# Optimization experiments

Hardware: AMD Instinct MI355X
Metric: run time of the kernel (lower is better)

Reference implementation:

```python
import jax, jax.numpy as jnp
import numpy as np

TWO_PI = 2.0 * np.pi
B, S_IN, S_OUT, K, HID = 1024, 4096, 4096, 8, 512
EPS = 1e-6


def setup_inputs() -> dict:
    key = jax.random.key(0)
    k1, k2, k3, k4, k5, k6, k7, k8 = jax.random.split(key, 8)
    x_in = jax.random.uniform(k1, (B, S_OUT), dtype=jnp.float32) * TWO_PI
    x_passive = jax.random.normal(k2, (B, S_IN), dtype=jnp.float32)
    log_density = jax.random.normal(k3, (B, 1), dtype=jnp.float32)
    # MLP params (nn.Linear default-ish init scale)
    lim1 = 1.0 / np.sqrt(S_IN)
    lim2 = 1.0 / np.sqrt(HID)
    w1 = jax.random.uniform(k4, (S_IN, HID), jnp.float32, -lim1, lim1)
    b1 = jax.random.uniform(k5, (HID,), jnp.float32, -lim1, lim1)
    w2 = jax.random.uniform(k6, (HID, S_OUT * 3 * K), jnp.float32, -lim2, lim2)
    b2 = jax.random.uniform(k7, (S_OUT * 3 * K,), jnp.float32, -lim2, lim2)
    phase_shift = jax.random.uniform(k8, (1,), jnp.float32)
    return {"x_in": x_in, "x_passive": x_passive, "log_density": log_density,
            "w1": w1, "b1": b1, "w2": w2, "b2": b2, "phase_shift": phase_shift}


def reference(x_in, x_passive, log_density, w1, b1, w2, b2, phase_shift):
    # normalise network input with global mean / (unbiased) std, as torch does
    xn = (x_passive - x_passive.mean()) / x_passive.std(ddof=1)
    # dense network: Linear -> tanh -> Linear -> tanh (final_activation=activation)
    net = jnp.tanh(jnp.tanh(xn @ w1 + b1) @ w2 + b2)            # (B, S*3K)
    net = net.reshape(-1, S_OUT, 3 * K)
    h_raw, w_raw, d_raw = net[..., :K], net[..., K:2 * K], net[..., 2 * K:]
    h_norm = jax.nn.softmax(h_raw, axis=2) * TWO_PI              # (B,S,K)
    w_norm = jax.nn.softmax(w_raw, axis=2) * TWO_PI
    d_norm = jax.nn.softplus(d_raw)
    bshape = (h_norm.shape[0], S_OUT, 1)
    x_kp = jnp.concatenate([jnp.full(bshape, -EPS, h_norm.dtype),
                            jnp.cumsum(w_norm, axis=2)], axis=2)  # (B,S,K+1)
    phi_kp = jnp.concatenate([jnp.zeros(bshape, h_norm.dtype),
                              jnp.cumsum(h_norm, axis=2)], axis=2)
    x = x_in[..., None]                                          # (B,S,1)
    # searchsorted (left) per element: count of knots strictly less than x, minus 1
    k_ind = jnp.sum(x_kp < x, axis=2, keepdims=True) - 1         # (B,S,1) int
    k_ind = jnp.clip(k_ind, 0, K - 1)
    g = lambda a, i: jnp.take_along_axis(a, i, axis=2)
    w_k = g(w_norm, k_ind)
    h_k = g(h_norm, k_ind)
    s_k = h_k / w_k
    d_k = g(d_norm, k_ind)
    d_kp1 = g(d_norm, (k_ind + 1) % K)
    x_km1 = g(x_kp, k_ind)
    phi_km1 = g(phi_kp, k_ind)
    alpha = (x - x_km1) / w_k
    a1m = alpha * (1.0 - alpha)
    denom = s_k + (d_kp1 + d_k - 2.0 * s_k) * a1m
    phi_out = (phi_km1 + h_k * (s_k * alpha ** 2 + d_k * a1m) / denom)[..., 0]
    phi_out = (phi_out + phase_shift) % TWO_PI                   # (B,S)
    grad = s_k ** 2 * (d_kp1 * alpha ** 2 + 2.0 * s_k * a1m
                       + d_k * (1.0 - alpha) ** 2) / denom ** 2  # (B,S,1)
    log_density = log_density - jnp.log(grad).sum(axis=1)        # (B,1)
    return phi_out, log_density
```

## Files before the change

### kernel.cpp

```cpp
#include <hip/hip_runtime.h>
#include <cstdint>
#include <cstddef>


typedef unsigned short u16;
typedef __bf16 bf16x8 __attribute__((ext_vector_type(8)));
typedef float f32x4 __attribute__((ext_vector_type(4)));
typedef unsigned short u16x8 __attribute__((ext_vector_type(8)));
typedef unsigned short u16x4 __attribute__((ext_vector_type(4)));
typedef unsigned short u16x2 __attribute__((ext_vector_type(2)));

#define TWOPI_F 6.28318530717958647692f

static __device__ __forceinline__ u16 f32_to_bf16(float f){
  unsigned u = __builtin_bit_cast(unsigned, f);
  return (u16)((u + 0x7fffu + ((u >> 16) & 1u)) >> 16);
}
static __device__ __forceinline__ void async16(void* lds, const void* g){
  __builtin_amdgcn_global_load_lds((const __attribute__((address_space(1))) void*)g,
                                   (__attribute__((address_space(3))) void*)lds,
                                   16, 0, 0);
}
static __device__ __forceinline__ float rcpf(float x){ return __builtin_amdgcn_rcpf(x); }
static __device__ __forceinline__ float fast_tanh(float x){
  x = fminf(fmaxf(x, -15.f), 15.f);
  float e = __expf(2.f * x);
  return (e - 1.f) / (e + 1.f);
}
static __device__ __forceinline__ float tanh_nc(float x){
  const float e2 = __expf(2.f * x);
  return 1.f - 2.f * rcpf(e2 + 1.f);
}
static __device__ __forceinline__ float exp_tanh(float x){
  const float e2 = __expf(2.f * x);
  const float u  = rcpf(e2 + 1.f);
  return __expf(1.f - 2.f * u);
}

__global__ void k_stats(const float* __restrict__ xp, float* __restrict__ stats){
  __shared__ float ss[4], sq[4];
  const int tid = threadIdx.x;
  const long gt = (long)blockIdx.x * 256 + tid;
  const float4* x4 = (const float4*)xp;
  float s = 0.f, q = 0.f;
  #pragma unroll
  for (int p = 0; p < 4; ++p){
    float4 v = x4[gt + (long)p * 262144];
    s += v.x + v.y + v.z + v.w;
    q += v.x*v.x + v.y*v.y + v.z*v.z + v.w*v.w;
  }
  #pragma unroll
  for (int off = 32; off; off >>= 1){
    s += __shfl_down(s, off);
    q += __shfl_down(q, off);
  }
  if ((tid & 63) == 0){ ss[tid>>6] = s; sq[tid>>6] = q; }
  __syncthreads();
  if (tid == 0){
    atomicAdd(stats,     ss[0]+ss[1]+ss[2]+ss[3]);
    atomicAdd(stats + 1, sq[0]+sq[1]+sq[2]+sq[3]);
  }
}

__global__ void k_prep(const float* __restrict__ xp, const float* __restrict__ stats,
                       u16* __restrict__ xn){
  const long t = (long)blockIdx.x * 256 + threadIdx.x;
  const float sum = stats[0], sq = stats[1];
  const float N = 4194304.f;
  const float mean = sum / N;
  const float istd = rsqrtf((sq - sum*sum/N) / (N - 1.f));
  const float4* x4 = (const float4*)xp;
  const float4 a = x4[2*t], b = x4[2*t+1];
  u16x8 o;
  o[0]=f32_to_bf16((a.x-mean)*istd); o[1]=f32_to_bf16((a.y-mean)*istd);
  o[2]=f32_to_bf16((a.z-mean)*istd); o[3]=f32_to_bf16((a.w-mean)*istd);
  o[4]=f32_to_bf16((b.x-mean)*istd); o[5]=f32_to_bf16((b.y-mean)*istd);
  o[6]=f32_to_bf16((b.z-mean)*istd); o[7]=f32_to_bf16((b.w-mean)*istd);
  ((u16x8*)xn)[t] = o;
}

__global__ __launch_bounds__(256) void k_transpose_cvt(const float* __restrict__ in,
                                                       u16* __restrict__ out,
                                                       int Kd, int Nd){
  __shared__ __align__(16) u16 tT[128*256];
  const int tid = threadIdx.x;
  const long k0 = (long)blockIdx.x * 256, n0 = (long)blockIdx.y * 128;
  const int lam = tid & 31, g = tid >> 5;
  const int c = lam * 4;
  const int sig = (lam & 7) << 2;
  #pragma unroll
  for (int pass = 0; pass < 16; ++pass){
    const int P = pass*8 + g;
    const float4 f0 = *(const float4*)&in[(k0 + 2*P    )*Nd + n0 + c];
    const float4 f1 = *(const float4*)&in[(k0 + 2*P + 1)*Nd + n0 + c];
    const int pp = 2*(P ^ sig);
    *(u16x2*)&tT[(c    )*256 + pp] = u16x2{f32_to_bf16(f0.x), f32_to_bf16(f1.x)};
    *(u16x2*)&tT[(c + 1)*256 + pp] = u16x2{f32_to_bf16(f0.y), f32_to_bf16(f1.y)};
    *(u16x2*)&tT[(c + 2)*256 + pp] = u16x2{f32_to_bf16(f0.z), f32_to_bf16(f1.z)};
    *(u16x2*)&tT[(c + 3)*256 + pp] = u16x2{f32_to_bf16(f0.w), f32_to_bf16(f1.w)};
  }
  __syncthreads();
  const int w = tid >> 6, l = tid & 63;
  const int lh = l >> 5, lk = l & 31;
  #pragma unroll
  for (int it = 0; it < 16; ++it){
    const int n = (w << 5) + (it << 1) + lh;
    const int s2 = (n >> 2) & 7;
    const u16x8 v = *(const u16x8*)&tT[n*256 + 8*(lk ^ s2)];
    *(u16x8*)&out[(n0 + n)*Kd + k0 + 8*lk] = v;
  }
}

__global__ __launch_bounds__(256, 2) void k_gemm1(
    const u16* __restrict__ xn,
    const u16* __restrict__ w1t,
    float* __restrict__ pp)
{
  __shared__ __align__(16) u16 sA[4][64*32];
  __shared__ __align__(16) u16 sB[4][64*32];
  const int tid = threadIdx.x, lane = tid & 63, w = tid >> 6;
  const int n0 = blockIdx.x << 6, m0 = blockIdx.y << 6;
  const int ks = blockIdx.z;
  const int wm = w >> 1, wn = w & 1;
  const int rA = lane >> 2, cA = (lane & 3) << 3;
  const int fr = lane & 15, fq = lane >> 4;
  const f32x4 z4 = {0.f, 0.f, 0.f, 0.f};
  f32x4 acc[2][2];
  #pragma unroll
  for (int i=0;i<2;i++){ acc[i][0] = z4; acc[i][1] = z4; }

  auto stage = [&](int kt){
    const int b = kt & 3;
    const int kofs = (ks << 11) + (kt << 5) + cA;
    async16(sA[b] + w*512, xn  + (long)(m0 + w*16 + rA)*4096 + kofs);
    async16(sB[b] + w*512, w1t + (long)(n0 + w*16 + rA)*4096 + kofs);
  };

  stage(0); stage(1);
  for (int kt = 0; kt < 64; ++kt){
    if (kt < 62){
      stage(kt + 2);
      asm volatile("s_waitcnt vmcnt(4)" ::: "memory");
    } else if (kt == 62){
      asm volatile("s_waitcnt vmcnt(2)" ::: "memory");
    } else {
      asm volatile("s_waitcnt vmcnt(0)" ::: "memory");
    }
    __builtin_amdgcn_s_barrier();
    const int b = kt & 3;
    bf16x8 af[2], bfv[2];
    #pragma unroll
    for (int i=0;i<2;i++) af[i]  = *(const bf16x8*)(sA[b] + ((wm<<5) + i*16 + fr)*32 + (fq<<3));
    #pragma unroll
    for (int j=0;j<2;j++) bfv[j] = *(const bf16x8*)(sB[b] + ((wn<<5) + j*16 + fr)*32 + (fq<<3));
    #pragma unroll
    for (int i=0;i<2;i++)
      #pragma unroll
      for (int j=0;j<2;j++)
        acc[i][j] = __builtin_amdgcn_mfma_f32_16x16x32_bf16(af[i], bfv[j], acc[i][j], 0, 0, 0);
  }
  float* po = pp + ((size_t)ks << 19);
  #pragma unroll
  for (int i=0;i<2;i++)
    #pragma unroll
    for (int j=0;j<2;j++)
      #pragma unroll
      for (int r=0;r<4;r++){
        const int row = m0 + (wm<<5) + i*16 + (fq<<2) + r;
        const int col = n0 + (wn<<5) + j*16 + fr;
        po[row*512 + col] = acc[i][j][r];
      }
}

__global__ void k_gemm1b(const float* __restrict__ pp, const float* __restrict__ b1,
                         u16* __restrict__ hb){
  const int t = blockIdx.x * 256 + threadIdx.x;
  const float4 a = ((const float4*)pp)[t];
  const float4 b = ((const float4*)pp)[131072 + t];
  const float4 bb = ((const float4*)b1)[t & 127];
  u16x4 o;
  o[0] = f32_to_bf16(fast_tanh(a.x + b.x + bb.x));
  o[1] = f32_to_bf16(fast_tanh(a.y + b.y + bb.y));
  o[2] = f32_to_bf16(fast_tanh(a.z + b.z + bb.z));
  o[3] = f32_to_bf16(fast_tanh(a.w + b.w + bb.w));
  ((u16x4*)hb)[t] = o;
}

__global__ __launch_bounds__(256, 2) void k_gemm2(
    const u16* __restrict__ hmat,
    const u16* __restrict__ w2t,
    const float* __restrict__ b2,
    const float* __restrict__ x_in,
    const float* __restrict__ phase,
    float* __restrict__ phi_out,
    float* __restrict__ part)
{
  __shared__ __align__(16) char smem[25600];
  u16* sA = (u16*)smem;
  u16* sB = (u16*)(smem + 16384);
  float* sC = (float*)smem;

  const int tid  = threadIdx.x;
  const int lane = tid & 63;
  const int w    = tid >> 6;
  const int id   = blockIdx.x;
  const int work = ((id & 7) << 9) | (id >> 3);
  const int m0   = (work & 3) << 8;
  const int nt   = work >> 2;
  const long n0  = (long)nt * 96;

  const int rA = lane >> 2, cA = (lane & 3) << 3;
  const int fr = lane & 15, fq = lane >> 4;

  const f32x4 z4 = {0.f, 0.f, 0.f, 0.f};
  f32x4 acc[4][6];
  #pragma unroll
  for (int i=0;i<4;i++)
    #pragma unroll
    for (int j=0;j<6;j++) acc[i][j] = z4;

  auto stage = [&](int kt){
    const int kofs = (kt << 5) + cA;
    #pragma unroll
    for (int cc = 0; cc < 4; ++cc){
      const int c = (w << 2) + cc;
      async16(sA + c*512, hmat + (long)(m0 + c*16 + rA)*512 + kofs);
    }
    #pragma unroll
    for (int cc = 0; cc < 2; ++cc){
      const int ch = (w << 1) + cc;
      int row = ch*16 + rA; if (row > 95) row = 95;
      async16(sB + ch*512, w2t + (n0 + row)*512 + kofs);
    }
  };

  stage(0);
  for (int kt = 0; kt < 16; ++kt){
    asm volatile("s_waitcnt vmcnt(0)" ::: "memory");
    __builtin_amdgcn_s_barrier();
    bf16x8 af[4], bfv[6];
    #pragma unroll
    for (int i=0;i<4;i++)
      af[i] = *(const bf16x8*)(sA + ((w<<6) + i*16 + fr)*32 + (fq<<3));
    #pragma unroll
    for (int j=0;j<6;j++)
      bfv[j] = *(const bf16x8*)(sB + (j*16 + fr)*32 + (fq<<3));
    asm volatile("s_waitcnt lgkmcnt(0)" ::: "memory");
    __builtin_amdgcn_sched_barrier(0);
    __builtin_amdgcn_s_barrier();
    if (kt < 15) stage(kt + 1);
    __builtin_amdgcn_sched_barrier(0);
    #pragma unroll
    for (int i=0;i<4;i++)
      #pragma unroll
      for (int j=0;j<6;j++)
        acc[i][j] = __builtin_amdgcn_mfma_f32_16x16x32_bf16(af[i], bfv[j], acc[i][j], 0, 0, 0);
  }

  const float shift = phase[0];
  float b2c[6];
  #pragma unroll
  for (int j=0;j<6;j++) b2c[j] = b2[n0 + j*16 + fr];
  float* myC = sC + w*1600;

  #pragma unroll
  for (int q = 0; q < 4; ++q){
    #pragma unroll
    for (int j=0;j<6;j++)
      #pragma unroll
      for (int r=0;r<4;r++)
        myC[((fq<<2)+r)*100 + j*16 + fr] = acc[q][j][r] + b2c[j];

    const int row = fr;
    const int g   = fq;
    const float* tp = myC + row*100 + g*24;
    float t[16];
    #pragma unroll
    for (int jj=0;jj<4;jj++){
      const f32x4 v = *(const f32x4*)(tp + 4*jj);
      t[4*jj] = v[0]; t[4*jj+1] = v[1]; t[4*jj+2] = v[2]; t[4*jj+3] = v[3];
    }

    const int bg = m0 + (w<<6) + (q<<4) + row;
    const int s  = (nt<<2) + g;
    const float x = x_in[(long)bg*4096 + s];

    float eh[8], ew[8];
    float sh = 0.f, sw = 0.f;
    #pragma unroll
    for (int i=0;i<8;i++){ eh[i] = exp_tanh(t[i]);   sh += eh[i]; }
    #pragma unroll
    for (int i=0;i<8;i++){ ew[i] = exp_tanh(t[8+i]); sw += ew[i]; }

    const float xs = x * sw * (1.f / TWOPI_F);
    float cw = 0.f; int k = 0;
    #pragma unroll
    for (int i=0;i<8;i++){ cw += ew[i]; k += (cw < xs) ? 1 : 0; }
    if (k > 7) k = 7;

    float wkr = 0.f, hkr = 0.f, xkr = 0.f, phr = 0.f;
    float c2 = 0.f, h2 = 0.f;
    #pragma unroll
    for (int i=0;i<8;i++){
      if (i == k){ wkr = ew[i]; hkr = eh[i]; xkr = c2; phr = h2; }
      c2 += ew[i]; h2 += eh[i];
    }

    const float* dp = tp + 16;
    const float th0 = tanh_nc(dp[k]);
    const float th1 = tanh_nc(dp[(k + 1) & 7]);
    const float dk  = __logf(1.f + __expf(th0));
    const float dk1 = __logf(1.f + __expf(th1));

    const float rsh = rcpf(sh);
    const float rwk = rcpf(wkr);
    const float alpha = (xs - xkr) * rwk;
    const float sk = hkr * rwk * (sw * rsh);
    const float hk = TWOPI_F * hkr * rsh;
    const float ph = TWOPI_F * phr * rsh;
    const float a1m = alpha * (1.f - alpha);
    const float denom = sk + (dk1 + dk - 2.f*sk)*a1m;
    const float rd = rcpf(denom);
    const float phiv = ph + hk*(sk*alpha*alpha + dk*a1m)*rd;
    float p = phiv + shift;
    if (p >= TWOPI_F) p -= TWOPI_F;
    if (p >= TWOPI_F) p -= TWOPI_F;
    phi_out[(long)bg*4096 + s] = p;

    const float om = 1.f - alpha;
    const float num = dk1*alpha*alpha + 2.f*sk*a1m + dk*om*om;
    const float srd = sk * rd;
    float lg = __logf(srd*srd*num);
    lg += __shfl_xor(lg, 16);
    lg += __shfl_xor(lg, 32);
    if (lane < 16) part[(long)bg*1024 + nt] = lg;
  }
}

__global__ void k_ldred(const float* __restrict__ part, const float* __restrict__ ldin,
                        float* __restrict__ ldout){
  __shared__ float ss[4];
  const int b = blockIdx.x, tid = threadIdx.x;
  const float4* p4 = (const float4*)(part + ((long)b << 10));
  const float4 v = p4[tid];
  float s = v.x + v.y + v.z + v.w;
  #pragma unroll
  for (int off = 32; off; off >>= 1) s += __shfl_down(s, off);
  if ((tid & 63) == 0) ss[tid >> 6] = s;
  __syncthreads();
  if (tid == 0) ldout[b] = ldin[b] - (ss[0]+ss[1]+ss[2]+ss[3]);
}

extern "C" void kernel_launch(void* const* d_in, const int* in_sizes, int n_in,
                              void* d_out, int out_size, void* d_ws, size_t ws_size,
                              hipStream_t stream){
  (void)in_sizes; (void)n_in; (void)out_size; (void)ws_size;
  const float* x_in  = (const float*)d_in[0];
  const float* x_pas = (const float*)d_in[1];
  const float* ldin  = (const float*)d_in[2];
  const float* w1    = (const float*)d_in[3];
  const float* b1    = (const float*)d_in[4];
  const float* w2    = (const float*)d_in[5];
  const float* b2    = (const float*)d_in[6];
  const float* phase = (const float*)d_in[7];
  float* out   = (float*)d_out;
  float* phi   = out;
  float* ldout = out + (size_t)1024*4096;

  char* ws = (char*)d_ws;
  float* stats = (float*)ws;
  u16* xn   = (u16*)(ws + 256);
  u16* w1t  = (u16*)(ws + 8388864);
  u16* hb   = (u16*)(ws + 12583168);
  u16* w2t  = (u16*)(ws + 13631744);
  float* part = (float*)(ws + 114295040);

  hipMemsetAsync(stats, 0, 8, stream);
  k_stats<<<1024, 256, 0, stream>>>(x_pas, stats);
  k_prep<<<2048, 256, 0, stream>>>(x_pas, stats, xn);
  k_transpose_cvt<<<dim3(16, 4),  256, 0, stream>>>(w1, w1t, 4096, 512);
  k_transpose_cvt<<<dim3(2, 768), 256, 0, stream>>>(w2, w2t, 512, 98304);
  k_gemm1<<<dim3(8, 16, 2), 256, 0, stream>>>(xn, w1t, part);
  k_gemm1b<<<512, 256, 0, stream>>>(part, b1, hb);
  k_gemm2<<<dim3(4096), 256, 0, stream>>>(hb, w2t, b2, x_in, phase, phi, part);
  k_ldred<<<1024, 256, 0, stream>>>(part, ldin, ldout);
}
```

Before: 532.5 us.

## Use 32x32x16 MFMA with swizzled LDS and fuse log-density reduction via atomics

Switches the second GEMM from 16x16x32 to 32x32x16 bf16 MFMA tiles, with an XOR swizzle on the LDS layout to avoid bank conflicts, and remaps the accumulator epilogue to the new register layout. It also drops the separate log-density reduction kernel: k_stats copies the input log-density to the output, and the GEMM epilogue atomically subtracts partial log sums. This trades fewer LDS reads and MFMA issues plus one fewer launch for atomic contention and a reduction order that is no longer deterministic.

Measured after the change: 562.6 us. 5.7% more time.

```diff
diff --git a/kernel.cpp b/kernel.cpp
--- a/kernel.cpp
+++ b/kernel.cpp
@@ -6,6 +6,7 @@
 typedef unsigned short u16;
 typedef __bf16 bf16x8 __attribute__((ext_vector_type(8)));
 typedef float f32x4 __attribute__((ext_vector_type(4)));
+typedef float f32x16 __attribute__((ext_vector_type(16)));
 typedef unsigned short u16x8 __attribute__((ext_vector_type(8)));
 typedef unsigned short u16x4 __attribute__((ext_vector_type(4)));
 typedef unsigned short u16x2 __attribute__((ext_vector_type(2)));
@@ -37,9 +38,11 @@
   return __expf(1.f - 2.f * u);
 }
 
-__global__ void k_stats(const float* __restrict__ xp, float* __restrict__ stats){
+__global__ void k_stats(const float* __restrict__ xp, float* __restrict__ stats,
+                        const float* __restrict__ ldin, float* __restrict__ ldout){
   __shared__ float ss[4], sq[4];
   const int tid = threadIdx.x;
+  if (tid == 0) ldout[blockIdx.x] = ldin[blockIdx.x];
   const long gt = (long)blockIdx.x * 256 + tid;
   const float4* x4 = (const float4*)xp;
   float s = 0.f, q = 0.f;
@@ -193,7 +196,7 @@
     const float* __restrict__ x_in,
     const float* __restrict__ phase,
     float* __restrict__ phi_out,
-    float* __restrict__ part)
+    float* __restrict__ ld)
 {
   __shared__ __align__(16) char smem[25600];
   u16* sA = (u16*)smem;
@@ -209,18 +212,22 @@
   const int nt   = work >> 2;
   const long n0  = (long)nt * 96;
 
-  const int rA = lane >> 2, cA = (lane & 3) << 3;
-  const int fr = lane & 15, fq = lane >> 4;
-
-  const f32x4 z4 = {0.f, 0.f, 0.f, 0.f};
-  f32x4 acc[4][6];
-  #pragma unroll
-  for (int i=0;i<4;i++)
-    #pragma unroll
-    for (int j=0;j<6;j++) acc[i][j] = z4;
+  const int rA  = lane >> 2;
+  const int cAs = (((lane & 3) ^ ((lane >> 3) & 3)) << 3);
+  const int lr  = lane & 31, hi = lane >> 5;
+  const int rho = (lr >> 1) & 3;
+  const int fr  = lane & 15, fq = lane >> 4;
+
+  f32x16 acc[2][3];
+  #pragma unroll
+  for (int i=0;i<2;i++)
+    #pragma unroll
+    for (int j=0;j<3;j++)
+      #pragma unroll
+      for (int r=0;r<16;r++) acc[i][j][r] = 0.f;
 
   auto stage = [&](int kt){
-    const int kofs = (kt << 5) + cA;
+    const int kofs = (kt << 5) + cAs;
     #pragma unroll
     for (int cc = 0; cc < 4; ++cc){
       const int c = (w << 2) + cc;
@@ -238,38 +245,48 @@
   for (int kt = 0; kt < 16; ++kt){
     asm volatile("s_waitcnt vmcnt(0)" ::: "memory");
     __builtin_amdgcn_s_barrier();
-    bf16x8 af[4], bfv[6];
-    #pragma unroll
-    for (int i=0;i<4;i++)
-      af[i] = *(const bf16x8*)(sA + ((w<<6) + i*16 + fr)*32 + (fq<<3));
-    #pragma unroll
-    for (int j=0;j<6;j++)
-      bfv[j] = *(const bf16x8*)(sB + (j*16 + fr)*32 + (fq<<3));
+    bf16x8 af[2][2], bfv[3][2];
+    #pragma unroll
+    for (int rb=0; rb<2; ++rb)
+      #pragma unroll
+      for (int kh=0; kh<2; ++kh)
+        af[rb][kh] = *(const bf16x8*)(sA + ((w<<6) + rb*32 + lr)*32 + ((((kh<<1)|hi) ^ rho)<<3));
+    #pragma unroll
+    for (int cb=0; cb<3; ++cb)
+      #pragma unroll
+      for (int kh=0; kh<2; ++kh)
+        bfv[cb][kh] = *(const bf16x8*)(sB + (cb*32 + lr)*32 + ((((kh<<1)|hi) ^ rho)<<3));
     asm volatile("s_waitcnt lgkmcnt(0)" ::: "memory");
     __builtin_amdgcn_sched_barrier(0);
     __builtin_amdgcn_s_barrier();
     if (kt < 15) stage(kt + 1);
     __builtin_amdgcn_sched_barrier(0);
     #pragma unroll
-    for (int i=0;i<4;i++)
-      #pragma unroll
-      for (int j=0;j<6;j++)
-        acc[i][j] = __builtin_amdgcn_mfma_f32_16x16x32_bf16(af[i], bfv[j], acc[i][j], 0, 0, 0);
+    for (int rb=0; rb<2; ++rb)
+      #pragma unroll
+      for (int cb=0; cb<3; ++cb){
+        acc[rb][cb] = __builtin_amdgcn_mfma_f32_32x32x16_bf16(af[rb][0], bfv[cb][0], acc[rb][cb], 0, 0, 0);
+        acc[rb][cb] = __builtin_amdgcn_mfma_f32_32x32x16_bf16(af[rb][1], bfv[cb][1], acc[rb][cb], 0, 0, 0);
+      }
   }
 
   const float shift = phase[0];
-  float b2c[6];
-  #pragma unroll
-  for (int j=0;j<6;j++) b2c[j] = b2[n0 + j*16 + fr];
+  float b2c[3];
+  #pragma unroll
+  for (int cb=0;cb<3;cb++) b2c[cb] = b2[n0 + cb*32 + lr];
   float* myC = sC + w*1600;
 
   #pragma unroll
   for (int q = 0; q < 4; ++q){
-    #pragma unroll
-    for (int j=0;j<6;j++)
-      #pragma unroll
-      for (int r=0;r<4;r++)
-        myC[((fq<<2)+r)*100 + j*16 + fr] = acc[q][j][r] + b2c[j];
+    const int rb = q >> 1;
+    #pragma unroll
+    for (int cb=0;cb<3;++cb)
+      #pragma unroll
+      for (int rr=0;rr<8;++rr){
+        const int r = ((q & 1) << 3) + rr;
+        const int row16 = (rr & 3) + (hi << 2) + ((rr >> 2) << 3);
+        myC[row16*100 + cb*32 + lr] = acc[rb][cb][r] + b2c[cb];
+      }
 
     const int row = fr;
     const int g   = fq;
@@ -333,22 +350,8 @@
     float lg = __logf(srd*srd*num);
     lg += __shfl_xor(lg, 16);
     lg += __shfl_xor(lg, 32);
-    if (lane < 16) part[(long)bg*1024 + nt] = lg;
-  }
-}
-
-__global__ void k_ldred(const float* __restrict__ part, const float* __restrict__ ldin,
-                        float* __restrict__ ldout){
-  __shared__ float ss[4];
-  const int b = blockIdx.x, tid = threadIdx.x;
-  const float4* p4 = (const float4*)(part + ((long)b << 10));
-  const float4 v = p4[tid];
-  float s = v.x + v.y + v.z + v.w;
-  #pragma unroll
-  for (int off = 32; off; off >>= 1) s += __shfl_down(s, off);
-  if ((tid & 63) == 0) ss[tid >> 6] = s;
-  __syncthreads();
-  if (tid == 0) ldout[b] = ldin[b] - (ss[0]+ss[1]+ss[2]+ss[3]);
+    if (lane < 16) atomicAdd(ld + bg, -lg);
+  }
 }
 
 extern "C" void kernel_launch(void* const* d_in, const int* in_sizes, int n_in,
@@ -376,12 +379,11 @@
   float* part = (float*)(ws + 114295040);
 
   hipMemsetAsync(stats, 0, 8, stream);
-  k_stats<<<1024, 256, 0, stream>>>(x_pas, stats);
+  k_stats<<<1024, 256, 0, stream>>>(x_pas, stats, ldin, ldout);
   k_prep<<<2048, 256, 0, stream>>>(x_pas, stats, xn);
   k_transpose_cvt<<<dim3(16, 4),  256, 0, stream>>>(w1, w1t, 4096, 512);
   k_transpose_cvt<<<dim3(2, 768), 256, 0, stream>>>(w2, w2t, 512, 98304);
   k_gemm1<<<dim3(8, 16, 2), 256, 0, stream>>>(xn, w1t, part);
   k_gemm1b<<<512, 256, 0, stream>>>(part, b1, hb);
-  k_gemm2<<<dim3(4096), 256, 0, stream>>>(hb, w2t, b2, x_in, phase, phi, part);
-  k_ldred<<<1024, 256, 0, stream>>>(part, ldin, ldout);
-}
+  k_gemm2<<<dim3(4096), 256, 0, stream>>>(hb, w2t, b2, x_in, phase, phi, ldout);
+}
```
